# Performance work log

Hardware: AMD Instinct MI355X
Metric: run time of the kernel (lower is better)

Reference implementation:

```python
import jax, jax.numpy as jnp
import numpy as np

BATCH, IN, HID, OMID, OUT = 8192, 64, 1024, 128, 1
MAX_ITER = 8
EPS = 1e-3


def setup_inputs() -> dict:
    key = jax.random.key(0)
    ks = jax.random.split(key, 32)
    s_in, s_h = 1.0 / np.sqrt(IN), 1.0 / np.sqrt(HID)
    d = {"x": jax.random.normal(ks[0], (BATCH, IN), jnp.float32)}
    names = ["i", "f", "c", "o"]
    for j, n in enumerate(names):
        d[f"Wx{n}"] = jax.random.uniform(ks[1 + 4 * j], (HID, IN), jnp.float32, -s_in, s_in)
        d[f"bx{n}"] = jax.random.uniform(ks[2 + 4 * j], (HID,), jnp.float32, -s_in, s_in)
        d[f"Wh{n}"] = jax.random.uniform(ks[3 + 4 * j], (HID, HID), jnp.float32, -s_h, s_h)
        d[f"bh{n}"] = jax.random.uniform(ks[4 + 4 * j], (HID,), jnp.float32, -s_h, s_h)
    d["W_halt"] = jax.random.uniform(ks[20], (1, HID), jnp.float32, -s_h, s_h)
    d["b_halt"] = jax.random.uniform(ks[21], (1,), jnp.float32, -s_h, s_h)
    d["W1"] = jax.random.uniform(ks[22], (OMID, HID), jnp.float32, -s_h, s_h)
    d["b1"] = jax.random.uniform(ks[23], (OMID,), jnp.float32, -s_h, s_h)
    s_m = 1.0 / np.sqrt(OMID)
    d["W2"] = jax.random.uniform(ks[24], (OUT, OMID), jnp.float32, -s_m, s_m)
    d["b2"] = jax.random.uniform(ks[25], (OUT,), jnp.float32, -s_m, s_m)
    return d


def _act_forward(x, Wxi, bxi, Whi, bhi, Wxf, bxf, Whf, bhf, Wxc, bxc, Whc, bhc,
                 Wxo, bxo, Who, bho, W_halt, b_halt, W1, b1, W2, b2):
    B = x.shape[0]
    state0 = jnp.zeros((B, HID), x.dtype)
    cell0 = jnp.zeros((B, HID), x.dtype)
    p0 = jnp.zeros((B,), x.dtype)
    active0 = jnp.ones((B,), bool)

    def step(carry, t):
        state, cell, p_sum, active = carry
        # four LSTM-style gates (computed dense; masked update == torch's gather/scatter)
        i_g = jax.nn.sigmoid(x @ Wxi.T + bxi + state @ Whi.T + bhi)
        f_g = jax.nn.sigmoid(x @ Wxf.T + bxf + state @ Whf.T + bhf)
        c_g = jnp.tanh(x @ Wxc.T + bxc + state @ Whc.T + bhc)
        o_g = jax.nn.sigmoid(x @ Wxo.T + bxo + state @ Who.T + bho)
        am = active[:, None]
        cell = jnp.where(am, f_g * cell + i_g * c_g, cell)
        state = jnp.where(am, o_g * jnp.tanh(cell), state)
        out = jax.nn.sigmoid(jax.nn.relu(state @ W1.T + b1) @ W2.T + b2)  # (B, OUT)
        h = jax.nn.sigmoid(state @ W_halt.T + b_halt)[:, 0]               # (B,)
        p_new = p_sum + h
        last = t == MAX_ITER - 1
        finished = active & ((p_new >= 1.0 - EPS) | last)
        halt_rec = jnp.where(finished, 1.0 - p_sum, jnp.where(active, h, 0.0))
        p_sum = jnp.where(finished, 1.0, jnp.where(active, p_new, p_sum))
        out_rec = jnp.where(am, out, 0.0)
        active = active & ~finished
        return (state, cell, p_sum, active), (out_rec, halt_rec)

    _, (outs, halts) = jax.lax.scan(step, (state0, cell0, p0, active0), jnp.arange(MAX_ITER))
    # outs: (T, B, OUT), halts: (T, B); final = sum_t out_t * p_halt_t
    return jnp.einsum("tbo,tb->bo", outs, halts)


def reference(x, Wxi, bxi, Whi, bhi, Wxf, bxf, Whf, bhf, Wxc, bxc, Whc, bhc,
              Wxo, bxo, Who, bho, W_halt, b_halt, W1, b1, W2, b2):
    return _act_forward(x, Wxi, bxi, Whi, bhi, Wxf, bxf, Whf, bhf, Wxc, bxc, Whc, bhc,
                        Wxo, bxo, Who, bho, W_halt, b_halt, W1, b1, W2, b2)
```

## Files before the change

### kernel.cpp

```cpp
#include <hip/hip_runtime.h>
#include <hip/hip_bf16.h>

#define BATCH 8192
#define IN_DIM 64
#define HID 1024
#define KTOT 1088
#define NGATES 4096
#define OMID 128
#define NP 256
#define MAX_ITER 8

#define TM 128
#define TN 128
#define TK 64
#define TMF 16
#define NBH 144
#define GTM 256
#define GTN 256
#define TAILB 64

typedef __attribute__((ext_vector_type(8))) short short8;
typedef __attribute__((ext_vector_type(4))) float float4v;
typedef __attribute__((ext_vector_type(4))) float float4f;
typedef __attribute__((ext_vector_type(4))) short short4v;

__device__ __forceinline__ float bf2f(short s) {
    union { float f; unsigned u; } v; v.u = ((unsigned)(unsigned short)s) << 16; return v.f;
}
__device__ __forceinline__ short f2bf(float f) {
    union { float f; unsigned u; } v; v.f = f;
    unsigned r = v.u + 0x7fff + ((v.u >> 16) & 1);
    return (short)(r >> 16);
}
__device__ __forceinline__ float sigmoidf_(float x) {
    float xc = fminf(fmaxf(x, -30.f), 30.f);
    return 1.f / (1.f + __expf(-xc));
}
__device__ __forceinline__ float tanhf_(float x) {
    float xc = fminf(fmaxf(x, -15.f), 15.f);
    float e = __expf(2.f * xc);
    return (e - 1.f) / (e + 1.f);
}
__device__ __forceinline__ int aload(const int* p) {
    return __hip_atomic_load((int*)p, __ATOMIC_RELAXED, __HIP_MEMORY_SCOPE_AGENT);
}
__device__ __forceinline__ void astore(int* p, int v) {
    __hip_atomic_store(p, v, __ATOMIC_RELAXED, __HIP_MEMORY_SCOPE_AGENT);
}

__device__ __forceinline__ void gbar(int* bar, int phase, int tid) {
    __syncthreads();
    if (tid == 0) {
        __threadfence();
        __hip_atomic_fetch_add(bar, 1, __ATOMIC_ACQ_REL, __HIP_MEMORY_SCOPE_AGENT);
        while (aload(bar) < TAILB * phase)
            __builtin_amdgcn_s_sleep(8);
        __threadfence();
    }
    __syncthreads();
}

__device__ __forceinline__ void gates_epilogue(
    const float4v (&acc)[4][4], int m0, int bx, int wave, int lane, int first,
    const float* __restrict__ bias_g, float* __restrict__ cell,
    short* __restrict__ Sout, const int* __restrict__ ridx, int n_act)
{
    const int wm = wave & 1, wn = wave >> 1;
    const int colq = lane & 15, q = lane >> 4;
    const int G = bx * 2 + wn;
    const int h = G * 16 + colq;
    const float bi  = bias_g[G * 64 +  0 + colq];
    const float bff = bias_g[G * 64 + 16 + colq];
    const float bc  = bias_g[G * 64 + 32 + colq];
    const float bo  = bias_g[G * 64 + 48 + colq];
#pragma unroll
    for (int i = 0; i < 4; ++i) {
        const int pbase = m0 + wm * 64 + i * 16 + q * 4;
#pragma unroll
        for (int r = 0; r < 4; ++r) {
            const int pos = pbase + r;
            if (pos < n_act) {
                const int row = ridx[pos];
                const float ig = sigmoidf_(acc[i][0][r] + bi);
                const float fg = sigmoidf_(acc[i][1][r] + bff);
                const float cg = tanhf_(acc[i][2][r] + bc);
                const float og = sigmoidf_(acc[i][3][r] + bo);
                const size_t ci = (size_t)row * HID + h;
                const float c = first ? (ig * cg) : (fg * cell[ci] + ig * cg);
                cell[ci] = c;
                Sout[(size_t)row * HID + h] = f2bf(og * tanhf_(c));
            }
        }
    }
}

__global__ __launch_bounds__(512, 1) void gates_k(
    const short* __restrict__ S, const short* __restrict__ XB,
    const short* __restrict__ B,
    const float* __restrict__ bias_g, int nK, int hidK, int first,
    float* __restrict__ cell, short* __restrict__ Sout,
    const int* __restrict__ ridx, const int* __restrict__ cnt, int t)
{
    __shared__ short As[2][GTM * TK];
    __shared__ short Bs[2][GTN * TK];
    const int n_act = cnt[t];
    const int tid  = threadIdx.x;
    const int wave = tid >> 6, lane = tid & 63;
    const int wm2 = wave >> 2, wn4 = wave & 3;
    const int colq = lane & 15, q = lane >> 4;
    const int lrow8 = lane >> 3;
    const int lk    = (((lane & 7) ^ lrow8) * 8);
    const int xq = colq & 7;
    const int abase = (wm2 * 128 + colq) * TK;
    const int bbase = (wn4 * 64  + colq) * TK;

    int bx, byS;
    {
        const int lin  = (int)blockIdx.x + 16 * (int)blockIdx.y;
        const int xcd  = lin & 7;
        const int slot = lin >> 3;
        bx  = (xcd & 1) * 8 + (slot & 7);
        byS = (xcd >> 1) * 4 + (slot >> 3);
    }
    const int n0 = bx * GTN;

    for (int by = byS; by * GTM < n_act; by += 16) {
        const int m0 = by * GTM;

        int rows_[4];
        const short* gb[4];
#pragma unroll
        for (int it = 0; it < 4; ++it) {
            const int rr = wave * 32 + it * 8 + lrow8;
            rows_[it] = ridx[m0 + rr];
            gb[it] = B + (size_t)(n0 + rr) * KTOT + lk;
        }

        float4v acc[8][4];
#pragma unroll
        for (int i = 0; i < 8; ++i)
#pragma unroll
            for (int j = 0; j < 4; ++j) acc[i][j] = (float4v)0.f;

        auto stage = [&](int ki, int buf) {
            const int kk = ki * TK;
            const bool fromS = (kk < hidK);
#pragma unroll
            for (int it = 0; it < 4; ++it) {
                const int dst = (wave * 32 + it * 8) * TK;
                const short* sa = fromS
                    ? (S  + (size_t)rows_[it] * HID    + kk + lk)
                    : (XB + (size_t)rows_[it] * IN_DIM + lk);
                __builtin_amdgcn_global_load_lds(
                    (const __attribute__((address_space(1))) void*)sa,
                    (__attribute__((address_space(3))) void*)(As[buf] + dst), 16, 0, 0);
                __builtin_amdgcn_global_load_lds(
                    (const __attribute__((address_space(1))) void*)(gb[it] + kk),
                    (__attribute__((address_space(3))) void*)(Bs[buf] + dst), 16, 0, 0);
            }
        };

        stage(0, 0);
        __syncthreads();

        for (int ki = 0; ki < nK; ++ki) {
            const int cur = ki & 1;
            if (ki + 1 < nK) stage(ki + 1, cur ^ 1);
            const short* Ac = As[cur];
            const short* Bc = Bs[cur];
#pragma unroll
            for (int c2 = 0; c2 < 2; ++c2) {
                const int xt = ((q + 4 * c2) ^ xq) << 3;
                short8 af[8], bf[4];
#pragma unroll
                for (int i = 0; i < 8; ++i)
                    af[i] = *(const short8*)(Ac + abase + i * (16 * TK) + xt);
#pragma unroll
                for (int j = 0; j < 4; ++j)
                    bf[j] = *(const short8*)(Bc + bbase + j * (16 * TK) + xt);
#pragma unroll
                for (int i = 0; i < 8; ++i)
#pragma unroll
                    for (int j = 0; j < 4; ++j)
                        acc[i][j] = __builtin_amdgcn_mfma_f32_16x16x32_bf16(af[i], bf[j], acc[i][j], 0, 0, 0);
            }
            __syncthreads();
        }

        const int G = bx * 4 + wn4;
        const int h = G * 16 + colq;
        const float bi  = bias_g[G * 64 +  0 + colq];
        const float bff = bias_g[G * 64 + 16 + colq];
        const float bc  = bias_g[G * 64 + 32 + colq];
        const float bo  = bias_g[G * 64 + 48 + colq];
#pragma unroll
        for (int i = 0; i < 8; ++i) {
            const int pbase = m0 + wm2 * 128 + i * 16 + q * 4;
#pragma unroll
            for (int r = 0; r < 4; ++r) {
                const int pos = pbase + r;
                if (pos < n_act) {
                    const int row = ridx[pos];
                    const float ig = sigmoidf_(acc[i][0][r] + bi);
                    const float fg = sigmoidf_(acc[i][1][r] + bff);
                    const float cg = tanhf_(acc[i][2][r] + bc);
                    const float og = sigmoidf_(acc[i][3][r] + bo);
                    const size_t ci = (size_t)row * HID + h;
                    const float c = first ? (ig * cg) : (fg * cell[ci] + ig * cg);
                    cell[ci] = c;
                    Sout[(size_t)row * HID + h] = f2bf(og * tanhf_(c));
                }
            }
        }
    }
}

__device__ __forceinline__ void gates_tile(
    short* As, short* Bs, int tid,
    const short* __restrict__ S, const short* __restrict__ XB,
    const short* __restrict__ B,
    const float* __restrict__ bias_g,
    float* __restrict__ cell, short* __restrict__ Sout,
    const int* __restrict__ ridx, int n_act, int m0, int bx)
{
    const int wave = tid >> 6, lane = tid & 63;
    const int wm = wave & 1, wn = wave >> 1;
    const int colq = lane & 15, q = lane >> 4;
    const int lrow8 = lane >> 3;
    const int lk    = (((lane & 7) ^ lrow8) * 8);
    const int n0 = bx * TN;

    int aoff[4][2], boff[4][2];
#pragma unroll
    for (int i = 0; i < 4; ++i) {
        const int Ra = wm * 64 + i * 16 + colq;
        const int Rb = wn * 64 + i * 16 + colq;
#pragma unroll
        for (int c2 = 0; c2 < 2; ++c2) {
            const int C = q + 4 * c2;
            aoff[i][c2] = Ra * TK + ((C ^ (Ra & 7)) << 3);
            boff[i][c2] = Rb * TK + ((C ^ (Rb & 7)) << 3);
        }
    }

    float4v acc[4][4];
#pragma unroll
    for (int i = 0; i < 4; ++i)
#pragma unroll
        for (int j = 0; j < 4; ++j) acc[i][j] = (float4v)0.f;

    const short* gaS[4];
    const short* gaX[4];
    const short* gb[4];
#pragma unroll
    for (int it = 0; it < 4; ++it) {
        const int rr = (wave * 4 + it) * 8;
        const int r0 = ridx[m0 + rr + lrow8];
        gaS[it] = S + (size_t)r0 * HID + lk;
        gaX[it] = XB + (size_t)r0 * IN_DIM + lk;
        gb[it]  = B + (size_t)(n0 + rr + lrow8) * KTOT + lk;
    }

    for (int ki = 0; ki < KTOT / TK; ++ki) {
        const bool fromS = (ki * TK < HID);
#pragma unroll
        for (int it = 0; it < 4; ++it) {
            const int rr = (wave * 4 + it) * 8;
            const short* a0 = fromS ? gaS[it] : gaX[it];
            __builtin_amdgcn_global_load_lds(
                (const __attribute__((address_space(1))) void*)a0,
                (__attribute__((address_space(3))) void*)(As + rr * TK), 16, 0, 0);
            __builtin_amdgcn_global_load_lds(
                (const __attribute__((address_space(1))) void*)gb[it],
                (__attribute__((address_space(3))) void*)(Bs + rr * TK), 16, 0, 0);
            gaS[it] += TK; gb[it] += TK;
        }
        __syncthreads();
#pragma unroll
        for (int c2 = 0; c2 < 2; ++c2) {
            short8 af[4], bf[4];
#pragma unroll
            for (int i = 0; i < 4; ++i) {
                af[i] = *(const short8*)(As + aoff[i][c2]);
                bf[i] = *(const short8*)(Bs + boff[i][c2]);
            }
#pragma unroll
            for (int i = 0; i < 4; ++i)
#pragma unroll
                for (int j = 0; j < 4; ++j)
                    acc[i][j] = __builtin_amdgcn_mfma_f32_16x16x32_bf16(af[i], bf[j], acc[i][j], 0, 0, 0);
        }
        __syncthreads();
    }

    gates_epilogue(acc, m0, bx, wave, lane, 0, bias_g, cell, Sout, ridx, n_act);
    __syncthreads();
}

__device__ __forceinline__ void midfin_tile(
    short* As0, short* As1, short* Bs0, short* Bs1, int tid,
    const short* __restrict__ Snew, const short* __restrict__ P,
    const float* __restrict__ bias_p, const float* __restrict__ W_halt,
    const float* __restrict__ W2, const float* __restrict__ b2,
    float* __restrict__ outp, float* __restrict__ p_sum,
    const int* __restrict__ rprev, int* __restrict__ rnext,
    int* __restrict__ cnt, int t, int m0, int n_act)
{
    const int wave = tid >> 6, lane = tid & 63;
    const int colq = lane & 15, q = lane >> 4;
    const int lrow8 = lane >> 3;
    const int lk    = (((lane & 7) ^ lrow8) * 8);
    const int xq = colq & 7;

    float4v acc[2];
    acc[0] = (float4v)0.f; acc[1] = (float4v)0.f;
    float4v acc_h = (float4v)0.f;

    const int arow_ = (wave < 2) ? rprev[m0 + wave * 8 + lrow8] : 0;
    const short* ga = Snew + (size_t)arow_ * HID + lk;
    const short* gbp[4];
#pragma unroll
    for (int g = 0; g < 4; ++g)
        gbp[g] = P + (size_t)(wave * 32 + g * 8 + lrow8) * HID + lk;
    const short* gbh[2];
#pragma unroll
    for (int l = 0; l < 2; ++l)
        gbh[l] = P + (size_t)(128 + l * 8 + lrow8) * HID + lk;

    auto stage = [&](int ks, short* Asb, short* Bsb) {
        const int k0 = ks * TK;
        if (wave < 2)
            __builtin_amdgcn_global_load_lds(
                (const __attribute__((address_space(1))) void*)(ga + k0),
                (__attribute__((address_space(3))) void*)(Asb + (wave * 8) * TK), 16, 0, 0);
#pragma unroll
        for (int g = 0; g < 4; ++g)
            __builtin_amdgcn_global_load_lds(
                (const __attribute__((address_space(1))) void*)(gbp[g] + k0),
                (__attribute__((address_space(3))) void*)(Bsb + (wave * 32 + g * 8) * TK), 16, 0, 0);
        if (wave == 3)
#pragma unroll
            for (int l = 0; l < 2; ++l)
                __builtin_amdgcn_global_load_lds(
                    (const __attribute__((address_space(1))) void*)(gbh[l] + k0),
                    (__attribute__((address_space(3))) void*)(Bsb + (128 + l * 8) * TK), 16, 0, 0);
    };

    stage(0, As0, Bs0);
    __syncthreads();

    for (int ks = 0; ks < HID / TK; ++ks) {
        const int cur = ks & 1;
        if (ks + 1 < HID / TK)
            stage(ks + 1, cur ? As0 : As1, cur ? Bs0 : Bs1);
        const short* Asb = cur ? As1 : As0;
        const short* Bsb = cur ? Bs1 : Bs0;
#pragma unroll
        for (int c2 = 0; c2 < 2; ++c2) {
            const int xt = ((q + 4 * c2) ^ xq) << 3;
            const short8 af = *(const short8*)(Asb + colq * TK + xt);
            const short8 bf0 = *(const short8*)(Bsb + (wave * 32 + colq) * TK + xt);
            const short8 bf1 = *(const short8*)(Bsb + (wave * 32 + 16 + colq) * TK + xt);
            acc[0] = __builtin_amdgcn_mfma_f32_16x16x32_bf16(af, bf0, acc[0], 0, 0, 0);
            acc[1] = __builtin_amdgcn_mfma_f32_16x16x32_bf16(af, bf1, acc[1], 0, 0, 0);
            if (wave == 0) {
                const short8 bh = *(const short8*)(Bsb + (128 + colq) * TK + xt);
                acc_h = __builtin_amdgcn_mfma_f32_16x16x32_bf16(af, bh, acc_h, 0, 0, 0);
            }
        }
        __syncthreads();
    }

    float* red  = (float*)As0;
    float* hbuf = ((float*)As0) + 64;

    if (wave == 0 && colq == 0) {
#pragma unroll
        for (int r = 0; r < 4; ++r)
            hbuf[q * 4 + r] = acc_h[r];
    }

    float pr[4];
#pragma unroll
    for (int r = 0; r < 4; ++r) pr[r] = 0.f;
#pragma unroll
    for (int nj = 0; nj < 2; ++nj) {
        const int col = wave * 32 + nj * 16 + colq;
        const float b = bias_p[col];
        const float w2 = W2[col];
#pragma unroll
        for (int r = 0; r < 4; ++r)
            pr[r] += fmaxf(acc[nj][r] + b, 0.f) * w2;
    }
#pragma unroll
    for (int r = 0; r < 4; ++r) {
        float v = pr[r];
        v += __shfl_down(v, 8, 16);
        v += __shfl_down(v, 4, 16);
        v += __shfl_down(v, 2, 16);
        v += __shfl_down(v, 1, 16);
        if (colq == 0)
            red[(wave * 4 + q) * 4 + r] = v;
    }
    __syncthreads();

    if (tid < TMF) {
        const int pos = m0 + tid;
        if (pos < n_act) {
            const int lq = tid >> 2, r = tid & 3;
            float odot = 0.f;
#pragma unroll
            for (int w = 0; w < 4; ++w)
                odot += red[(w * 4 + lq) * 4 + r];
            const int row = rprev[pos];
            const float ov = sigmoidf_(odot + b2[0]);
            const float h  = sigmoidf_(hbuf[tid] + bias_p[OMID]);
            const float ps = p_sum[row];
            const float pn = ps + h;
            const bool fin = (pn >= 1.f - 1e-3f) || (t == MAX_ITER - 1);
            const float halt = fin ? (1.f - ps) : h;
            outp[row] += ov * halt;
            p_sum[row] = fin ? 1.f : pn;
            if (!fin) {
                const int d = atomicAdd(&cnt[t + 1], 1);
                astore(&rnext[d], row);
            }
        }
    }
    __syncthreads();
}

__global__ __launch_bounds__(256) void midfin_k(
    const short* __restrict__ Snew, const short* __restrict__ P,
    const float* __restrict__ bias_p, const float* __restrict__ W_halt,
    const float* __restrict__ W2, const float* __restrict__ b2,
    float* __restrict__ outp, float* __restrict__ p_sum,
    const int* __restrict__ rprev, int* __restrict__ rnext,
    int* __restrict__ cnt, int t)
{
    __shared__ short As[2][TMF * TK];
    __shared__ short Bs[2][NBH * TK];
    const int n_act = cnt[t];
    for (int tile = blockIdx.x; tile * TMF < n_act; tile += gridDim.x)
        midfin_tile(As[0], As[1], Bs[0], Bs[1], threadIdx.x,
                    Snew, P, bias_p, W_halt, W2, b2,
                    outp, p_sum, rprev, rnext, cnt, t, tile * TMF, n_act);
}

__global__ __launch_bounds__(256) void tail_k(
    const short* __restrict__ Wg, const float* __restrict__ bias_g,
    const short* __restrict__ P, const float* __restrict__ bias_p,
    const float* __restrict__ W_halt, const float* __restrict__ W2,
    const float* __restrict__ b2,
    short* __restrict__ S0, short* __restrict__ S1,
    const short* __restrict__ XB,
    float* __restrict__ cell, float* __restrict__ outp,
    float* __restrict__ p_sum,
    int* __restrict__ ridx0, int* __restrict__ ridx1,
    int* __restrict__ cnt, int* __restrict__ bar)
{
    __shared__ short As[2][TM * TK];
    __shared__ short Bs[2][NBH * TK];
    const int tid = threadIdx.x;
    int phase = 0;
    int t = 3;
    while (true) {
        short* Snew = (t & 1) ? S0 : S1;
        const int* rprev = (t & 1) ? ridx1 : ridx0;
        int* rnext = (t & 1) ? ridx0 : ridx1;
        const int n = aload(&cnt[t]);
        for (int tile = blockIdx.x; tile * TMF < n; tile += gridDim.x)
            midfin_tile(As[0], As[1], Bs[0], Bs[1], tid,
                        Snew, P, bias_p, W_halt, W2, b2,
                        outp, p_sum, rprev, rnext, cnt, t, tile * TMF, n);
        if (t == MAX_ITER - 1) break;
        ++phase; gbar(bar, phase, tid);
        const int n1 = aload(&cnt[t + 1]);
        if (n1 == 0) break;
        {
            short* Sot = (t & 1) ? S1 : S0;
            const int ntiles = ((n1 + TM - 1) / TM) * (NGATES / TN);
            for (int e = blockIdx.x; e < ntiles; e += gridDim.x)
                gates_tile(As[0], Bs[0], tid, Snew, XB, Wg, bias_g, cell, Sot,
                           rnext, n1, (e >> 5) * TM, e & 31);
        }
        ++phase; gbar(bar, phase, tid);
        ++t;
    }
}

#define SETUP_XB4   (BATCH * IN_DIM / 4)
#define SETUP_WG4   (NGATES * (KTOT / 4))
#define SETUP_P4    (NP * (HID / 4))
#define SETUP_TOT4  (SETUP_XB4 + SETUP_WG4 + SETUP_P4)
__global__ __launch_bounds__(256) void setup_k(
    const float* __restrict__ x,
    const float* __restrict__ Whi, const float* __restrict__ Whf,
    const float* __restrict__ Whc, const float* __restrict__ Who,
    const float* __restrict__ Wxi, const float* __restrict__ Wxf,
    const float* __restrict__ Wxc, const float* __restrict__ Wxo,
    const float* __restrict__ bxi, const float* __restrict__ bhi,
    const float* __restrict__ bxf, const float* __restrict__ bhf,
    const float* __restrict__ bxc, const float* __restrict__ bhc,
    const float* __restrict__ bxo, const float* __restrict__ bho,
    const float* __restrict__ W1, const float* __restrict__ b1,
    const float* __restrict__ W_halt, const float* __restrict__ b_halt,
    short* __restrict__ XB,
    float* __restrict__ p_sum,
    int* __restrict__ ridx0, int* __restrict__ ridx1, int* __restrict__ cnt,
    int* __restrict__ bar, float* __restrict__ outp,
    short* __restrict__ Wg, float* __restrict__ bias_g,
    short* __restrict__ P, float* __restrict__ bias_p)
{
    int idx = blockIdx.x * 256 + threadIdx.x;
    if (idx < SETUP_XB4) {
        const int row = idx >> 4, k4 = (idx & 15) * 4;
        const float4f v = *(const float4f*)(x + row * IN_DIM + k4);
        short4v o;
#pragma unroll
        for (int e = 0; e < 4; ++e) o[e] = f2bf(v[e]);
        *(short4v*)(XB + row * IN_DIM + k4) = o;
        if (k4 == 0) {
            p_sum[row] = 0.f;
            outp[row] = 0.f;
            ridx0[row] = row;
            ridx1[row] = 0;
        }
        if (idx == 0) {
            for (int k = 0; k <= MAX_ITER; ++k) cnt[k] = (k == 0) ? BATCH : 0;
            bar[0] = 0;
        }
        return;
    }
    idx -= SETUP_XB4;
    if (idx < SETUP_WG4) {
        const int n = idx / (KTOT / 4), k4 = (idx - n * (KTOT / 4)) * 4;
        const int G = n >> 6, g = (n >> 4) & 3, qq = n & 15;
        const int h = G * 16 + qq;
        const float* Wh = (g == 0) ? Whi : (g == 1) ? Whf : (g == 2) ? Whc : Who;
        const float* Wx = (g == 0) ? Wxi : (g == 1) ? Wxf : (g == 2) ? Wxc : Wxo;
        const float4f v = (k4 < HID)
            ? *(const float4f*)(Wh + h * HID + k4)
            : *(const float4f*)(Wx + h * IN_DIM + (k4 - HID));
        short4v o;
#pragma unroll
        for (int e = 0; e < 4; ++e) o[e] = f2bf(v[e]);
        *(short4v*)(Wg + (size_t)n * KTOT + k4) = o;
        if (k4 == 0) {
            const float* bx = (g == 0) ? bxi : (g == 1) ? bxf : (g == 2) ? bxc : bxo;
            const float* bh = (g == 0) ? bhi : (g == 1) ? bhf : (g == 2) ? bhc : bho;
            bias_g[n] = bx[h] + bh[h];
        }
        return;
    }
    idx -= SETUP_WG4;
    if (idx < SETUP_P4) {
        const int n = idx >> 8, k4 = (idx & 255) * 4;
        float4f v;
        if (n < OMID)      v = *(const float4f*)(W1 + n * HID + k4);
        else if (n == OMID) v = *(const float4f*)(W_halt + k4);
        else { v[0] = 0.f; v[1] = 0.f; v[2] = 0.f; v[3] = 0.f; }
        short4v o;
#pragma unroll
        for (int e = 0; e < 4; ++e) o[e] = f2bf(v[e]);
        *(short4v*)(P + (size_t)n * HID + k4) = o;
        if (k4 == 0) bias_p[n] = (n < OMID) ? b1[n] : (n == OMID ? b_halt[0] : 0.f);
    }
}

extern "C" void kernel_launch(void* const* d_in, const int* in_sizes, int n_in,
                              void* d_out, int out_size, void* d_ws, size_t ws_size,
                              hipStream_t stream) {
    const float* x    = (const float*)d_in[0];
    const float* Wxi  = (const float*)d_in[1];
    const float* bxi  = (const float*)d_in[2];
    const float* Whi  = (const float*)d_in[3];
    const float* bhi  = (const float*)d_in[4];
    const float* Wxf  = (const float*)d_in[5];
    const float* bxf  = (const float*)d_in[6];
    const float* Whf  = (const float*)d_in[7];
    const float* bhf  = (const float*)d_in[8];
    const float* Wxc  = (const float*)d_in[9];
    const float* bxc  = (const float*)d_in[10];
    const float* Whc  = (const float*)d_in[11];
    const float* bhc  = (const float*)d_in[12];
    const float* Wxo  = (const float*)d_in[13];
    const float* bxo  = (const float*)d_in[14];
    const float* Who  = (const float*)d_in[15];
    const float* bho  = (const float*)d_in[16];
    const float* W_halt = (const float*)d_in[17];
    const float* b_halt = (const float*)d_in[18];
    const float* W1   = (const float*)d_in[19];
    const float* b1   = (const float*)d_in[20];
    const float* W2   = (const float*)d_in[21];
    const float* b2   = (const float*)d_in[22];

    char* p = (char*)d_ws;
    auto carve = [&](size_t bytes) { char* r = p; p += (bytes + 255) & ~(size_t)255; return r; };
    short* S0     = (short*)carve((size_t)BATCH * HID * 2);
    short* S1     = (short*)carve((size_t)BATCH * HID * 2);
    short* XB     = (short*)carve((size_t)BATCH * IN_DIM * 2);
    short* Wg     = (short*)carve((size_t)NGATES * KTOT * 2);
    float* bias_g = (float*)carve((size_t)NGATES * 4);
    short* P      = (short*)carve((size_t)NP * HID * 2);
    float* bias_p = (float*)carve((size_t)NP * 4);
    float* cell   = (float*)carve((size_t)BATCH * HID * 4);
    float* p_sum  = (float*)carve((size_t)BATCH * 4);
    int*   ridx0  = (int*)carve((size_t)BATCH * 4);
    int*   ridx1  = (int*)carve((size_t)BATCH * 4);
    int*   cnt    = (int*)carve((size_t)(MAX_ITER + 1) * 4);
    int*   bar    = (int*)carve(256);
    float* outp   = (float*)d_out;

    setup_k<<<(SETUP_TOT4 + 255) / 256, 256, 0, stream>>>(
        x, Whi, Whf, Whc, Who, Wxi, Wxf, Wxc, Wxo,
        bxi, bhi, bxf, bhf, bxc, bhc, bxo, bho,
        W1, b1, W_halt, b_halt,
        XB, p_sum, ridx0, ridx1, cnt, bar, outp,
        Wg, bias_g, P, bias_p);

    gates_k<<<dim3(16, 16), 512, 0, stream>>>(
        S0, XB, Wg + HID, bias_g, 1, 0, 1, cell, S1, ridx0, cnt, 0);
    midfin_k<<<512, 256, 0, stream>>>(
        S1, P, bias_p, W_halt, W2, b2, outp, p_sum, ridx0, ridx1, cnt, 0);
    gates_k<<<dim3(16, 16), 512, 0, stream>>>(
        S1, XB, Wg, bias_g, KTOT / TK, HID, 0, cell, S0, ridx1, cnt, 1);
    midfin_k<<<512, 256, 0, stream>>>(
        S0, P, bias_p, W_halt, W2, b2, outp, p_sum, ridx1, ridx0, cnt, 1);
    gates_k<<<dim3(16, 16), 512, 0, stream>>>(
        S0, XB, Wg, bias_g, KTOT / TK, HID, 0, cell, S1, ridx0, cnt, 2);
    midfin_k<<<512, 256, 0, stream>>>(
        S1, P, bias_p, W_halt, W2, b2, outp, p_sum, ridx0, ridx1, cnt, 2);
    tail_k<<<TAILB, 256, 0, stream>>>(
        Wg, bias_g, P, bias_p, W_halt, W2, b2,
        S0, S1, XB, cell, outp, p_sum, ridx0, ridx1, cnt, bar);
}
```

Baseline: 405.3 us.

## Shrink gates GEMM tile to 128x128 and read weight fragments directly from global

The gates kernel moves from 256x256 tiles with 512 threads to 128x128 tiles with 256 threads on a 32x64 grid. Only the gathered activation rows are staged through shared memory, while the weight B fragments are loaded straight from global memory (served by L2/L1) into registers. The epilogue moves into a shared gates_epilogue helper. This cuts LDS use and raises occupancy and the number of blocks, but gives up reuse of staged B tiles and puts uncoalesced-ish global loads inside the MFMA loop.

```diff
diff --git a/kernel.cpp b/kernel.cpp
--- a/kernel.cpp
+++ b/kernel.cpp
@@ -15,8 +15,6 @@
 #define TK 64
 #define TMF 16
 #define NBH 144
-#define GTM 256
-#define GTN 256
 #define TAILB 64
 
 typedef __attribute__((ext_vector_type(8))) short short8;
@@ -94,51 +92,55 @@
     }
 }
 
-__global__ __launch_bounds__(512, 1) void gates_k(
+__global__ __launch_bounds__(256) void gates_k(
     const short* __restrict__ S, const short* __restrict__ XB,
     const short* __restrict__ B,
     const float* __restrict__ bias_g, int nK, int hidK, int first,
     float* __restrict__ cell, short* __restrict__ Sout,
     const int* __restrict__ ridx, const int* __restrict__ cnt, int t)
 {
-    __shared__ short As[2][GTM * TK];
-    __shared__ short Bs[2][GTN * TK];
+    __shared__ short As[2][TM * TK];
     const int n_act = cnt[t];
     const int tid  = threadIdx.x;
     const int wave = tid >> 6, lane = tid & 63;
-    const int wm2 = wave >> 2, wn4 = wave & 3;
+    const int wm = wave & 1, wn = wave >> 1;
     const int colq = lane & 15, q = lane >> 4;
     const int lrow8 = lane >> 3;
     const int lk    = (((lane & 7) ^ lrow8) * 8);
     const int xq = colq & 7;
-    const int abase = (wm2 * 128 + colq) * TK;
-    const int bbase = (wn4 * 64  + colq) * TK;
 
     int bx, byS;
     {
-        const int lin  = (int)blockIdx.x + 16 * (int)blockIdx.y;
+        const int lin  = (int)blockIdx.x + 32 * (int)blockIdx.y;
         const int xcd  = lin & 7;
         const int slot = lin >> 3;
-        bx  = (xcd & 1) * 8 + (slot & 7);
-        byS = (xcd >> 1) * 4 + (slot >> 3);
-    }
-    const int n0 = bx * GTN;
-
-    for (int by = byS; by * GTM < n_act; by += 16) {
-        const int m0 = by * GTM;
+        bx  = xcd * 4 + (slot & 3);
+        byS = slot >> 2;
+    }
+    const int n0 = bx * TN;
+
+    const short* Bg = B + (size_t)(n0 + wn * 64 + colq) * KTOT + q * 8;
+
+    int aoff[4][2];
+#pragma unroll
+    for (int i = 0; i < 4; ++i) {
+        const int Ra = wm * 64 + i * 16 + colq;
+#pragma unroll
+        for (int c2 = 0; c2 < 2; ++c2)
+            aoff[i][c2] = Ra * TK + (((q + 4 * c2) ^ xq) << 3);
+    }
+
+    for (int by = byS; by * TM < n_act; by += 64) {
+        const int m0 = by * TM;
 
         int rows_[4];
-        const short* gb[4];
-#pragma unroll
-        for (int it = 0; it < 4; ++it) {
-            const int rr = wave * 32 + it * 8 + lrow8;
-            rows_[it] = ridx[m0 + rr];
-            gb[it] = B + (size_t)(n0 + rr) * KTOT + lk;
-        }
-
-        float4v acc[8][4];
-#pragma unroll
-        for (int i = 0; i < 8; ++i)
+#pragma unroll
+        for (int it = 0; it < 4; ++it)
+            rows_[it] = ridx[m0 + wave * 32 + it * 8 + lrow8];
+
+        float4v acc[4][4];
+#pragma unroll
+        for (int i = 0; i < 4; ++i)
 #pragma unroll
             for (int j = 0; j < 4; ++j) acc[i][j] = (float4v)0.f;
 
@@ -154,9 +156,6 @@
                 __builtin_amdgcn_global_load_lds(
                     (const __attribute__((address_space(1))) void*)sa,
                     (__attribute__((address_space(3))) void*)(As[buf] + dst), 16, 0, 0);
-                __builtin_amdgcn_global_load_lds(
-                    (const __attribute__((address_space(1))) void*)(gb[it] + kk),
-                    (__attribute__((address_space(3))) void*)(Bs[buf] + dst), 16, 0, 0);
             }
         };
 
@@ -167,19 +166,18 @@
             const int cur = ki & 1;
             if (ki + 1 < nK) stage(ki + 1, cur ^ 1);
             const short* Ac = As[cur];
-            const short* Bc = Bs[cur];
+            const size_t kk = (size_t)ki * TK;
 #pragma unroll
             for (int c2 = 0; c2 < 2; ++c2) {
-                const int xt = ((q + 4 * c2) ^ xq) << 3;
-                short8 af[8], bf[4];
-#pragma unroll
-                for (int i = 0; i < 8; ++i)
-                    af[i] = *(const short8*)(Ac + abase + i * (16 * TK) + xt);
+                short8 af[4], bf[4];
+#pragma unroll
+                for (int i = 0; i < 4; ++i)
+                    af[i] = *(const short8*)(Ac + aoff[i][c2]);
 #pragma unroll
                 for (int j = 0; j < 4; ++j)
-                    bf[j] = *(const short8*)(Bc + bbase + j * (16 * TK) + xt);
-#pragma unroll
-                for (int i = 0; i < 8; ++i)
+                    bf[j] = *(const short8*)(Bg + (size_t)j * (16 * KTOT) + kk + c2 * 32);
+#pragma unroll
+                for (int i = 0; i < 4; ++i)
 #pragma unroll
                     for (int j = 0; j < 4; ++j)
                         acc[i][j] = __builtin_amdgcn_mfma_f32_16x16x32_bf16(af[i], bf[j], acc[i][j], 0, 0, 0);
@@ -187,31 +185,7 @@
             __syncthreads();
         }
 
-        const int G = bx * 4 + wn4;
-        const int h = G * 16 + colq;
-        const float bi  = bias_g[G * 64 +  0 + colq];
-        const float bff = bias_g[G * 64 + 16 + colq];
-        const float bc  = bias_g[G * 64 + 32 + colq];
-        const float bo  = bias_g[G * 64 + 48 + colq];
-#pragma unroll
-        for (int i = 0; i < 8; ++i) {
-            const int pbase = m0 + wm2 * 128 + i * 16 + q * 4;
-#pragma unroll
-            for (int r = 0; r < 4; ++r) {
-                const int pos = pbase + r;
-                if (pos < n_act) {
-                    const int row = ridx[pos];
-                    const float ig = sigmoidf_(acc[i][0][r] + bi);
-                    const float fg = sigmoidf_(acc[i][1][r] + bff);
-                    const float cg = tanhf_(acc[i][2][r] + bc);
-                    const float og = sigmoidf_(acc[i][3][r] + bo);
-                    const size_t ci = (size_t)row * HID + h;
-                    const float c = first ? (ig * cg) : (fg * cell[ci] + ig * cg);
-                    cell[ci] = c;
-                    Sout[(size_t)row * HID + h] = f2bf(og * tanhf_(c));
-                }
-            }
-        }
+        gates_epilogue(acc, m0, bx, wave, lane, first, bias_g, cell, Sout, ridx, n_act);
     }
 }
 
@@ -619,15 +593,15 @@
         XB, p_sum, ridx0, ridx1, cnt, bar, outp,
         Wg, bias_g, P, bias_p);
 
-    gates_k<<<dim3(16, 16), 512, 0, stream>>>(
+    gates_k<<<dim3(32, 64), 256, 0, stream>>>(
         S0, XB, Wg + HID, bias_g, 1, 0, 1, cell, S1, ridx0, cnt, 0);
     midfin_k<<<512, 256, 0, stream>>>(
         S1, P, bias_p, W_halt, W2, b2, outp, p_sum, ridx0, ridx1, cnt, 0);
-    gates_k<<<dim3(16, 16), 512, 0, stream>>>(
+    gates_k<<<dim3(32, 64), 256, 0, stream>>>(
         S1, XB, Wg, bias_g, KTOT / TK, HID, 0, cell, S0, ridx1, cnt, 1);
     midfin_k<<<512, 256, 0, stream>>>(
         S0, P, bias_p, W_halt, W2, b2, outp, p_sum, ridx1, ridx0, cnt, 1);
-    gates_k<<<dim3(16, 16), 512, 0, stream>>>(
+    gates_k<<<dim3(32, 64), 256, 0, stream>>>(
         S0, XB, Wg, bias_g, KTOT / TK, HID, 0, cell, S1, ridx0, cnt, 2);
     midfin_k<<<512, 256, 0, stream>>>(
         S1, P, bias_p, W_halt, W2, b2, outp, p_sum, ridx0, ridx1, cnt, 2);
```

New measurement: 464.5 us. 14.6% more time.
